# Kernel tuning notes

Measured on AMD Instinct MI355X. Metric: run time of the kernel, lower is better.

The kernel has to match this reference:

```python
import jax, jax.numpy as jnp
import numpy as np

EPS = 1e-5
K_SIZE, STRIDE, DILATION, N_HEADS = 8, 2, 2, 8


def ln2d(x, w, b):
    # LayerNorm2d: normalize over channel axis of NCHW
    m = x.mean(1, keepdims=True)
    v = x.var(1, keepdims=True)
    return (x - m) * jax.lax.rsqrt(v + EPS) * w[None, :, None, None] + b[None, :, None, None]


def setup_inputs() -> dict:
    key = jax.random.key(0)
    ks = jax.random.split(key, 8)
    B, C, H, W = 1, 64, 128, 128
    hid = 2 * C  # ffn_ratio = 2
    f = lambda k, s: jax.random.normal(k, s, jnp.float32) * 0.02
    return dict(
        x=jax.random.normal(ks[0], (B, C, H, W), jnp.float32),
        norm1_w=jnp.ones(C, jnp.float32), norm1_b=jnp.zeros(C, jnp.float32),
        qkv_w=f(ks[1], (3 * C, C)), qkv_b=jnp.zeros(3 * C, jnp.float32),
        qn_w=jnp.ones(C, jnp.float32), qn_b=jnp.zeros(C, jnp.float32),
        kn_w=jnp.ones(C, jnp.float32), kn_b=jnp.zeros(C, jnp.float32),
        proj_w=f(ks[2], (C, C)), proj_b=jnp.zeros(C, jnp.float32),
        gamma1=jnp.full((C,), 0.1, jnp.float32),
        norm2_w=jnp.ones(C, jnp.float32), norm2_b=jnp.zeros(C, jnp.float32),
        fc1_w=f(ks[3], (hid, C)), fc1_b=jnp.zeros(hid, jnp.float32),
        mn_w=jnp.ones(hid, jnp.float32), mn_b=jnp.zeros(hid, jnp.float32),
        fc2_w=f(ks[4], (C, hid)), fc2_b=jnp.zeros(C, jnp.float32),
        gamma2=jnp.full((C,), 0.1, jnp.float32),
    )


def reference(x, norm1_w, norm1_b, qkv_w, qkv_b, qn_w, qn_b, kn_w, kn_b,
              proj_w, proj_b, gamma1, norm2_w, norm2_b,
              fc1_w, fc1_b, mn_w, mn_b, fc2_w, fc2_b, gamma2):
    B, C, H, W = x.shape
    n = N_HEADS
    hd = C // n
    # strided + dilated neighborhood offsets (includes 0 at center)
    off = (jnp.arange(K_SIZE) * STRIDE - (K_SIZE * STRIDE) // 2) * DILATION

    # ---- neighborhood attention branch ----
    xn = ln2d(x, norm1_w, norm1_b)
    qkv = jnp.einsum('oc,bchw->bohw', qkv_w, xn) + qkv_b[None, :, None, None]
    q, k, v = jnp.split(qkv, 3, axis=1)
    q = ln2d(q, qn_w, qn_b)
    k = ln2d(k, kn_w, kn_b)
    q = q.reshape(B, n, hd, H, W)
    k = k.reshape(B, n, hd, H, W)
    v = v.reshape(B, n, hd, H, W)

    pos_h = jnp.arange(H)[:, None] + off[None, :]            # [H, k]
    vh = (pos_h >= 0) & (pos_h < H)
    ih = jnp.clip(pos_h, 0, H - 1)
    pos_w = jnp.arange(W)[:, None] + off[None, :]            # [W, k]
    vw = (pos_w >= 0) & (pos_w < W)
    iw = jnp.clip(pos_w, 0, W - 1)

    # gather neighborhoods: [B,n,hd,H,kh,W,kw]
    Kg = jnp.take(jnp.take(k, ih, axis=3), iw, axis=5)
    Vg = jnp.take(jnp.take(v, ih, axis=3), iw, axis=5)

    scores = jnp.einsum('bnchw,bnchiwj->bnhwij', q, Kg) * (hd ** -0.5)
    mask = vh[:, None, :, None] & vw[None, :, None, :]        # [H,W,kh,kw]
    scores = jnp.where(mask[None, None], scores, -jnp.inf)
    a = jax.nn.softmax(scores.reshape(B, n, H, W, -1), axis=-1).reshape(scores.shape)
    o = jnp.einsum('bnhwij,bnchiwj->bnchw', a, Vg).reshape(B, C, H, W)
    o = jnp.einsum('oc,bchw->bohw', proj_w, o) + proj_b[None, :, None, None]
    x = x + gamma1[None, :, None, None] * o                  # ls1 + residual (drop_path=0)

    # ---- ConvMlp branch: 1x1 conv -> norm -> silu -> 1x1 conv ----
    y = ln2d(x, norm2_w, norm2_b)
    h1 = jnp.einsum('oc,bchw->bohw', fc1_w, y) + fc1_b[None, :, None, None]
    h1 = jax.nn.silu(ln2d(h1, mn_w, mn_b))
    h2 = jnp.einsum('oc,bchw->bohw', fc2_w, h1) + fc2_b[None, :, None, None]
    return x + gamma2[None, :, None, None] * h2
```

## Files before the change

kernel.cpp:

```cpp
#include <hip/hip_runtime.h>
#include <math.h>

#define HW 16384
#define CC 64
#define HID 128
#define EPSV 1e-5f
#define ROW 36
#define SROW 69
#define HDSTR 131072

typedef __attribute__((ext_vector_type(8))) short bf16x8;
typedef __attribute__((ext_vector_type(4))) float f32x4v;

__device__ __forceinline__ unsigned short f2bf(float f) {
    unsigned u = __float_as_uint(f);
    u += 0x7FFFu + ((u >> 16) & 1u);
    return (unsigned short)(u >> 16);
}
__device__ __forceinline__ unsigned pack2bf(float a, float b) {
    return (unsigned)f2bf(a) | ((unsigned)f2bf(b) << 16);
}


__global__ __launch_bounds__(256) void k_ln_qkv(
    const float* __restrict__ x,
    const float* __restrict__ n1w, const float* __restrict__ n1b,
    const float* __restrict__ qkvw, const float* __restrict__ qkvb,
    const float* __restrict__ qnw, const float* __restrict__ qnb,
    const float* __restrict__ knw, const float* __restrict__ knb,
    float* __restrict__ qo, float* __restrict__ ko, float* __restrict__ vo)
{
    __shared__ __align__(16) float xs[CC][ROW];
    __shared__ __align__(16) float qk[32][SROW];
    __shared__ __align__(16) float mu1[32], rs1[32], mu2[32], rs2[32];

    const int t = threadIdx.x;
    const int pix0 = blockIdx.x * 32;
    const int sel = blockIdx.y;

    {
        const int c = t >> 2, pxq = (t & 3) * 8;
        *(float4*)&xs[c][pxq]     = *(const float4*)(x + c * HW + pix0 + pxq);
        *(float4*)&xs[c][pxq + 4] = *(const float4*)(x + c * HW + pix0 + pxq + 4);
    }
    __syncthreads();

    if (t < 128) {
        const int px = ((t >> 6) << 4) + (t & 15);
        const int part = (t & 63) >> 4;
        float s = 0.f, ss = 0.f;
        #pragma unroll
        for (int i = 0; i < 16; ++i) { float v = xs[part * 16 + i][px]; s += v; ss += v * v; }
        s += __shfl_xor(s, 16); ss += __shfl_xor(ss, 16);
        s += __shfl_xor(s, 32); ss += __shfl_xor(ss, 32);
        if (part == 0) {
            float m = s * (1.f / CC);
            mu1[px] = m;
            rs1[px] = rsqrtf(ss * (1.f / CC) - m * m + EPSV);
        }
    }
    __syncthreads();

    {
        const int c = t >> 2, pxq = (t & 3) * 8;
        const float wgt = n1w[c], bia = n1b[c];
        #pragma unroll
        for (int hh = 0; hh < 2; ++hh) {
            float4 v = *(float4*)&xs[c][pxq + hh * 4];
            float4 m4 = *(float4*)&mu1[pxq + hh * 4];
            float4 r4 = *(float4*)&rs1[pxq + hh * 4];
            v.x = (v.x - m4.x) * r4.x * wgt + bia;
            v.y = (v.y - m4.y) * r4.y * wgt + bia;
            v.z = (v.z - m4.z) * r4.z * wgt + bia;
            v.w = (v.w - m4.w) * r4.w * wgt + bia;
            *(float4*)&xs[c][pxq + hh * 4] = v;
        }
    }
    __syncthreads();

    {
        const int o0 = (t >> 3) * 2;
        const int px0 = (t & 7) * 4;
        const int ow = sel * 64 + o0;
        float a[2][4];
        #pragma unroll
        for (int j = 0; j < 2; ++j) {
            float b = qkvb[ow + j];
            a[j][0] = b; a[j][1] = b; a[j][2] = b; a[j][3] = b;
        }
        for (int c = 0; c < CC; c += 4) {
            float4 xv[4];
            #pragma unroll
            for (int i = 0; i < 4; ++i) xv[i] = *(float4*)&xs[c + i][px0];
            #pragma unroll
            for (int j = 0; j < 2; ++j) {
                float4 wv = *(const float4*)(qkvw + (ow + j) * CC + c);
                #pragma unroll
                for (int pp = 0; pp < 4; ++pp) {
                    a[j][pp] += wv.x * (&xv[0].x)[pp] + wv.y * (&xv[1].x)[pp]
                              + wv.z * (&xv[2].x)[pp] + wv.w * (&xv[3].x)[pp];
                }
            }
        }
        #pragma unroll
        for (int j = 0; j < 2; ++j) {
            #pragma unroll
            for (int pp = 0; pp < 4; ++pp) qk[px0 + pp][o0 + j] = a[j][pp];
        }
    }
    __syncthreads();

    if (sel < 2) {
        if (t < 128) {
            const int px = ((t >> 6) << 4) + (t & 15);
            const int part = (t & 63) >> 4;
            float s = 0.f, ss = 0.f;
            #pragma unroll
            for (int i = 0; i < 16; ++i) { float v = qk[px][part * 16 + i]; s += v; ss += v * v; }
            s += __shfl_xor(s, 16); ss += __shfl_xor(ss, 16);
            s += __shfl_xor(s, 32); ss += __shfl_xor(ss, 32);
            if (part == 0) {
                float m = s * (1.f / CC);
                mu2[px] = m;
                rs2[px] = rsqrtf(ss * (1.f / CC) - m * m + EPSV);
            }
        }
        __syncthreads();
    }

    const float* lw = (sel == 0) ? qnw : knw;
    const float* lb = (sel == 0) ? qnb : knb;
    float* dst = (sel == 0) ? qo : ((sel == 1) ? ko : vo);
    #pragma unroll
    for (int pass = 0; pass < 2; ++pass) {
        const int px = (t >> 4) + pass * 16;
        const int cg = t & 15;
        const int c = cg * 4;
        const int hd = cg >> 1;
        const int d4 = (cg & 1) * 4;
        const int pixel = pix0 + px;
        const int h = pixel >> 7, w = pixel & 127;
        const int pos = ((h >> 2) * 32 + (w >> 2)) * 16 + (h & 3) * 4 + (w & 3);
        const int gbase = hd * HDSTR + pos * 8 + d4;

        float4 vv = *(float4*)&qk[px][c];
        if (sel < 2) {
            const float mm = mu2[px], rr = rs2[px];
            float4 w4 = *(const float4*)(lw + c);
            float4 b4 = *(const float4*)(lb + c);
            vv.x = (vv.x - mm) * rr * w4.x + b4.x;
            vv.y = (vv.y - mm) * rr * w4.y + b4.y;
            vv.z = (vv.z - mm) * rr * w4.z + b4.z;
            vv.w = (vv.w - mm) * rr * w4.w + b4.w;
        }
        *(float4*)(dst + gbase) = vv;
    }
}

__global__ __launch_bounds__(256) void k_attn(
    const float* __restrict__ q, const float* __restrict__ k, const float* __restrict__ v,
    float* __restrict__ o,
    const float* __restrict__ pw, const float* __restrict__ f1w, const float* __restrict__ f2w,
    unsigned short* __restrict__ pwh, unsigned short* __restrict__ f1h,
    unsigned short* __restrict__ f2h)
{
    __shared__ __align__(16) float kt[4][15][33][2];
    __shared__ __align__(16) float vt[4][15][33][2];

    const int t = threadIdx.x;
    const int band = blockIdx.x;
    const int sub  = blockIdx.y;
    const int head = blockIdx.z;
    const int hs0 = band * 8;

    {
        const int gtid = ((blockIdx.z * 16 + blockIdx.y) * 4 + blockIdx.x) * 256 + t;
        if (gtid < 4096)        pwh[gtid] = f2bf(pw[gtid]);
        else if (gtid < 12288)  f1h[gtid - 4096] = f2bf(f1w[gtid - 4096]);
        else if (gtid < 20480)  f2h[gtid - 12288] = f2bf(f2w[gtid - 12288]);
    }

    const float* kb = k + head * HDSTR;
    const float* vb = v + head * HDSTR;

    for (int idx = t; idx < 960; idx += 256) {
        const int row = idx >> 6;
        const int rem = idx & 63;
        const int wsc = rem >> 1;
        const int dh = rem & 1;
        int gr = hs0 - 4 + row;
        gr = gr < 0 ? 0 : (gr > 31 ? 31 : gr);
        const int gaddr = ((gr * 32 + wsc) * 16 + sub) * 8 + dh * 4;
        const float4 kv4 = *(const float4*)(kb + gaddr);
        const float4 vv4 = *(const float4*)(vb + gaddr);
        const int dp = dh * 2;
        kt[dp][row][wsc][0] = kv4.x;     kt[dp][row][wsc][1] = kv4.y;
        kt[dp + 1][row][wsc][0] = kv4.z; kt[dp + 1][row][wsc][1] = kv4.w;
        vt[dp][row][wsc][0] = vv4.x;     vt[dp][row][wsc][1] = vv4.y;
        vt[dp + 1][row][wsc][0] = vv4.z; vt[dp + 1][row][wsc][1] = vv4.w;
    }

    const int r = t >> 5;
    const int wsc = t & 31;
    const int hs = hs0 + r;

    const float* qp = q + head * HDSTR + ((hs * 32 + wsc) * 16 + sub) * 8;
    const float4 q0 = *(const float4*)qp;
    const float4 q1 = *(const float4*)(qp + 4);
    const float scale = 0.35355339059327373f;

    __syncthreads();

    float s[64];
    float mx0 = -1e30f, mx1 = -1e30f, mx2 = -1e30f, mx3 = -1e30f;
    #pragma unroll
    for (int i = 0; i < 8; ++i) {
        const int lr = r + i;
        const bool vh = (unsigned)(hs + i - 4) < 32u;
        #pragma unroll
        for (int j = 0; j < 8; ++j) {
            const int cs = wsc + j - 4;
            const bool valid = vh && ((unsigned)cs < 32u);
            const int cc = cs < 0 ? 0 : (cs > 31 ? 31 : cs);
            const float2 kA = *(const float2*)&kt[0][lr][cc][0];
            const float2 kB = *(const float2*)&kt[1][lr][cc][0];
            const float2 kC = *(const float2*)&kt[2][lr][cc][0];
            const float2 kD = *(const float2*)&kt[3][lr][cc][0];
            float sv = q0.x * kA.x + q0.y * kA.y + q0.z * kB.x + q0.w * kB.y
                     + q1.x * kC.x + q1.y * kC.y + q1.z * kD.x + q1.w * kD.y;
            sv *= scale;
            sv = valid ? sv : -INFINITY;
            s[i * 8 + j] = sv;
            if ((j & 3) == 0)      mx0 = fmaxf(mx0, sv);
            else if ((j & 3) == 1) mx1 = fmaxf(mx1, sv);
            else if ((j & 3) == 2) mx2 = fmaxf(mx2, sv);
            else                   mx3 = fmaxf(mx3, sv);
        }
    }
    const float mx = fmaxf(fmaxf(mx0, mx1), fmaxf(mx2, mx3));

    float l = 0.f;
    float a0 = 0.f, a1 = 0.f, a2 = 0.f, a3 = 0.f, a4 = 0.f, a5 = 0.f, a6 = 0.f, a7 = 0.f;
    #pragma unroll
    for (int i = 0; i < 8; ++i) {
        const int lr = r + i;
        #pragma unroll
        for (int j = 0; j < 8; ++j) {
            const int cs = wsc + j - 4;
            const int cc = cs < 0 ? 0 : (cs > 31 ? 31 : cs);
            const float p = __expf(s[i * 8 + j] - mx);
            const float2 vA = *(const float2*)&vt[0][lr][cc][0];
            const float2 vB = *(const float2*)&vt[1][lr][cc][0];
            const float2 vC = *(const float2*)&vt[2][lr][cc][0];
            const float2 vD = *(const float2*)&vt[3][lr][cc][0];
            l += p;
            a0 += p * vA.x;  a1 += p * vA.y;
            a2 += p * vB.x;  a3 += p * vB.y;
            a4 += p * vC.x;  a5 += p * vC.y;
            a6 += p * vD.x;  a7 += p * vD.y;
        }
    }

    const float inv = 1.f / l;
    const int a = sub >> 2, b = sub & 3;
    const int h = hs * 4 + a, w = wsc * 4 + b;
    float* op = o + (h * 128 + w) * 64 + head * 8;
    float4 r0 = {a0 * inv, a1 * inv, a2 * inv, a3 * inv};
    float4 r1 = {a4 * inv, a5 * inv, a6 * inv, a7 * inv};
    *(float4*)op = r0;
    *(float4*)(op + 4) = r1;
}

__global__ __launch_bounds__(256) void k_mlp(
    const float* __restrict__ x, const float* __restrict__ oatt,
    const unsigned short* __restrict__ pwh, const float* __restrict__ pb,
    const float* __restrict__ g1,
    const float* __restrict__ n2w, const float* __restrict__ n2b,
    const unsigned short* __restrict__ f1h, const float* __restrict__ f1b,
    const float* __restrict__ mnw, const float* __restrict__ mnb,
    const unsigned short* __restrict__ f2h, const float* __restrict__ f2b,
    const float* __restrict__ g2,
    float* __restrict__ out)
{
    __shared__ __align__(16) float xres[CC][ROW];
    __shared__ __align__(16) unsigned short oh[32][72];
    __shared__ __align__(16) unsigned short tbh[32][72];
    __shared__ __align__(16) float h1[HID][ROW];
    __shared__ __align__(16) unsigned short h1h[32][136];
    __shared__ __align__(16) float mu[32], rs[32];

    const int t = threadIdx.x;
    const int pix0 = blockIdx.x * 32;
    const int wv = t >> 6;
    const int l = t & 63;
    const int ln = l & 15;
    const int kg = l >> 4;

    {
        const int c = t >> 2, pxq = (t & 3) * 8;
        *(float4*)&xres[c][pxq]     = *(const float4*)(x + c * HW + pix0 + pxq);
        *(float4*)&xres[c][pxq + 4] = *(const float4*)(x + c * HW + pix0 + pxq + 4);
    }
    #pragma unroll
    for (int pass = 0; pass < 2; ++pass) {
        const int px = (t >> 4) + pass * 16, cg = (t & 15) * 4;
        float4 ov = *(const float4*)(oatt + (pix0 + px) * CC + cg);
        *(unsigned*)&oh[px][cg]     = pack2bf(ov.x, ov.y);
        *(unsigned*)&oh[px][cg + 2] = pack2bf(ov.z, ov.w);
    }
    __syncthreads();

    {
        f32x4v acc0 = {0.f, 0.f, 0.f, 0.f}, acc1 = {0.f, 0.f, 0.f, 0.f};
        const int m = wv * 16 + ln;
        #pragma unroll
        for (int kk = 0; kk < 64; kk += 32) {
            const int k0 = kk + kg * 8;
            bf16x8 av = *(const bf16x8*)(pwh + m * 64 + k0);
            bf16x8 b0 = *(const bf16x8*)&oh[ln][k0];
            bf16x8 b1 = *(const bf16x8*)&oh[16 + ln][k0];
            acc0 = __builtin_amdgcn_mfma_f32_16x16x32_bf16(av, b0, acc0, 0, 0, 0);
            acc1 = __builtin_amdgcn_mfma_f32_16x16x32_bf16(av, b1, acc1, 0, 0, 0);
        }
        const int r0 = wv * 16 + kg * 4;
        float4 pb4 = *(const float4*)(pb + r0);
        float4 g14 = *(const float4*)(g1 + r0);
        #pragma unroll
        for (int reg = 0; reg < 4; ++reg) {
            const int row = r0 + reg;
            xres[row][ln]      += (&g14.x)[reg] * (acc0[reg] + (&pb4.x)[reg]);
            xres[row][16 + ln] += (&g14.x)[reg] * (acc1[reg] + (&pb4.x)[reg]);
        }
    }
    __syncthreads();

    if (t < 128) {
        const int px = ((t >> 6) << 4) + (t & 15);
        const int part = (t & 63) >> 4;
        float s = 0.f, ss = 0.f;
        #pragma unroll
        for (int i = 0; i < 16; ++i) { float v = xres[part * 16 + i][px]; s += v; ss += v * v; }
        s += __shfl_xor(s, 16); ss += __shfl_xor(ss, 16);
        s += __shfl_xor(s, 32); ss += __shfl_xor(ss, 32);
        if (part == 0) {
            float m = s * (1.f / CC);
            mu[px] = m;
            rs[px] = rsqrtf(ss * (1.f / CC) - m * m + EPSV);
        }
    }
    __syncthreads();

    {
        const int c2 = (t & 31) * 2, px0 = (t >> 5) * 4;
        const float w0 = n2w[c2], b0 = n2b[c2];
        const float w1 = n2w[c2 + 1], b1 = n2b[c2 + 1];
        float4 va = *(float4*)&xres[c2][px0];
        float4 vb = *(float4*)&xres[c2 + 1][px0];
        float4 m4 = *(float4*)&mu[px0];
        float4 r4 = *(float4*)&rs[px0];
        #pragma unroll
        for (int i = 0; i < 4; ++i) {
            float f0 = ((&va.x)[i] - (&m4.x)[i]) * (&r4.x)[i] * w0 + b0;
            float f1 = ((&vb.x)[i] - (&m4.x)[i]) * (&r4.x)[i] * w1 + b1;
            *(unsigned*)&tbh[px0 + i][c2] = pack2bf(f0, f1);
        }
    }
    __syncthreads();

    {
        f32x4v a00 = {0.f,0.f,0.f,0.f}, a01 = {0.f,0.f,0.f,0.f};
        f32x4v a10 = {0.f,0.f,0.f,0.f}, a11 = {0.f,0.f,0.f,0.f};
        const int m0 = wv * 32 + ln;
        #pragma unroll
        for (int kk = 0; kk < 64; kk += 32) {
            const int k0 = kk + kg * 8;
            bf16x8 av0 = *(const bf16x8*)(f1h + m0 * 64 + k0);
            bf16x8 av1 = *(const bf16x8*)(f1h + (m0 + 16) * 64 + k0);
            bf16x8 b0 = *(const bf16x8*)&tbh[ln][k0];
            bf16x8 b1 = *(const bf16x8*)&tbh[16 + ln][k0];
            a00 = __builtin_amdgcn_mfma_f32_16x16x32_bf16(av0, b0, a00, 0, 0, 0);
            a01 = __builtin_amdgcn_mfma_f32_16x16x32_bf16(av0, b1, a01, 0, 0, 0);
            a10 = __builtin_amdgcn_mfma_f32_16x16x32_bf16(av1, b0, a10, 0, 0, 0);
            a11 = __builtin_amdgcn_mfma_f32_16x16x32_bf16(av1, b1, a11, 0, 0, 0);
        }
        const int r0 = wv * 32 + kg * 4;
        float4 fb0 = *(const float4*)(f1b + r0);
        float4 fb1 = *(const float4*)(f1b + r0 + 16);
        #pragma unroll
        for (int reg = 0; reg < 4; ++reg) {
            h1[r0 + reg][ln]           = a00[reg] + (&fb0.x)[reg];
            h1[r0 + reg][16 + ln]      = a01[reg] + (&fb0.x)[reg];
            h1[r0 + 16 + reg][ln]      = a10[reg] + (&fb1.x)[reg];
            h1[r0 + 16 + reg][16 + ln] = a11[reg] + (&fb1.x)[reg];
        }
    }
    __syncthreads();

    if (t < 128) {
        const int px = ((t >> 6) << 4) + (t & 15);
        const int part = (t & 63) >> 4;
        float s = 0.f, ss = 0.f;
        #pragma unroll
        for (int i = 0; i < 32; ++i) { float v = h1[part * 32 + i][px]; s += v; ss += v * v; }
        s += __shfl_xor(s, 16); ss += __shfl_xor(ss, 16);
        s += __shfl_xor(s, 32); ss += __shfl_xor(ss, 32);
        if (part == 0) {
            float m = s * (1.f / HID);
            mu[px] = m;
            rs[px] = rsqrtf(ss * (1.f / HID) - m * m + EPSV);
        }
    }
    __syncthreads();

    {
        const int c2 = (t & 63) * 2, pxm = (t >> 6) * 8;
        const float w0 = mnw[c2], b0 = mnb[c2];
        const float w1 = mnw[c2 + 1], b1 = mnb[c2 + 1];
        #pragma unroll
        for (int qq = 0; qq < 2; ++qq) {
            float4 va = *(float4*)&h1[c2][pxm + qq * 4];
            float4 vb = *(float4*)&h1[c2 + 1][pxm + qq * 4];
            float4 m4 = *(float4*)&mu[pxm + qq * 4];
            float4 r4 = *(float4*)&rs[pxm + qq * 4];
            #pragma unroll
            for (int i = 0; i < 4; ++i) {
                float h0 = ((&va.x)[i] - (&m4.x)[i]) * (&r4.x)[i] * w0 + b0;
                float h1v = ((&vb.x)[i] - (&m4.x)[i]) * (&r4.x)[i] * w1 + b1;
                h0 = h0 / (1.f + __expf(-h0));
                h1v = h1v / (1.f + __expf(-h1v));
                *(unsigned*)&h1h[pxm + qq * 4 + i][c2] = pack2bf(h0, h1v);
            }
        }
    }
    __syncthreads();

    {
        f32x4v acc0 = {0.f, 0.f, 0.f, 0.f}, acc1 = {0.f, 0.f, 0.f, 0.f};
        const int m = wv * 16 + ln;
        #pragma unroll
        for (int kk = 0; kk < 128; kk += 32) {
            const int k0 = kk + kg * 8;
            bf16x8 av = *(const bf16x8*)(f2h + m * 128 + k0);
            bf16x8 b0 = *(const bf16x8*)&h1h[ln][k0];
            bf16x8 b1 = *(const bf16x8*)&h1h[16 + ln][k0];
            acc0 = __builtin_amdgcn_mfma_f32_16x16x32_bf16(av, b0, acc0, 0, 0, 0);
            acc1 = __builtin_amdgcn_mfma_f32_16x16x32_bf16(av, b1, acc1, 0, 0, 0);
        }
        const int r0 = wv * 16 + kg * 4;
        float4 fb4 = *(const float4*)(f2b + r0);
        float4 g24 = *(const float4*)(g2 + r0);
        #pragma unroll
        for (int reg = 0; reg < 4; ++reg) {
            const int row = r0 + reg;
            out[row * HW + pix0 + ln]      = xres[row][ln]
                                           + (&g24.x)[reg] * (acc0[reg] + (&fb4.x)[reg]);
            out[row * HW + pix0 + 16 + ln] = xres[row][16 + ln]
                                           + (&g24.x)[reg] * (acc1[reg] + (&fb4.x)[reg]);
        }
    }
}

extern "C" void kernel_launch(void* const* d_in, const int* in_sizes, int n_in,
                              void* d_out, int out_size, void* d_ws, size_t ws_size,
                              hipStream_t stream) {
    (void)in_sizes; (void)n_in; (void)out_size; (void)ws_size;
    const float* x      = (const float*)d_in[0];
    const float* n1w    = (const float*)d_in[1];
    const float* n1b    = (const float*)d_in[2];
    const float* qkvw   = (const float*)d_in[3];
    const float* qkvb   = (const float*)d_in[4];
    const float* qnw    = (const float*)d_in[5];
    const float* qnb    = (const float*)d_in[6];
    const float* knw    = (const float*)d_in[7];
    const float* knb    = (const float*)d_in[8];
    const float* pw     = (const float*)d_in[9];
    const float* pb     = (const float*)d_in[10];
    const float* g1     = (const float*)d_in[11];
    const float* n2w    = (const float*)d_in[12];
    const float* n2b    = (const float*)d_in[13];
    const float* f1w    = (const float*)d_in[14];
    const float* f1b    = (const float*)d_in[15];
    const float* mnw    = (const float*)d_in[16];
    const float* mnb    = (const float*)d_in[17];
    const float* f2w    = (const float*)d_in[18];
    const float* f2b    = (const float*)d_in[19];
    const float* g2     = (const float*)d_in[20];
    float* out = (float*)d_out;

    float* ws = (float*)d_ws;
    const size_t CHW = (size_t)CC * HW;
    float* qo   = ws;
    float* ko   = ws + CHW;
    float* vo   = ws + 2 * CHW;
    float* oatt = ws + 3 * CHW;
    unsigned short* wsh = (unsigned short*)(ws + 4 * CHW);
    unsigned short* pwh = wsh;
    unsigned short* f1h = wsh + 4096;
    unsigned short* f2h = wsh + 12288;

    k_ln_qkv<<<dim3(HW / 32, 3), dim3(256), 0, stream>>>(
        x, n1w, n1b, qkvw, qkvb, qnw, qnb, knw, knb, qo, ko, vo);
    k_attn<<<dim3(4, 16, 8), dim3(256), 0, stream>>>(
        qo, ko, vo, oatt, pw, f1w, f2w, pwh, f1h, f2h);
    k_mlp<<<dim3(HW / 32), dim3(256), 0, stream>>>(
        x, oatt, pwh, pb, g1, n2w, n2b, f1h, f1b, mnw, mnb, f2h, f2b, g2, out);
}
```

Before: 135.8 us.

## Compute QKV projection with bf16 MFMA in one block per pixel tile

The QKV kernel now computes all three 64-channel outputs in a single block rather than one block per q/k/v selector, so LayerNorm1 and the x tile load are no longer repeated three times. The 1x1 projection moves from fp32 FMA loops to bf16 MFMA 16x16x32 instructions, with weights and normalized activations converted to bf16 in shared memory. Both q and k LayerNorms run concurrently on separate halves of the block. The cost is more shared memory per block, lower occupancy, per-block weight conversion, and reduced precision in the projection.

```diff
diff --git a/kernel.cpp b/kernel.cpp
--- a/kernel.cpp
+++ b/kernel.cpp
@@ -6,7 +6,7 @@
 #define HID 128
 #define EPSV 1e-5f
 #define ROW 36
-#define SROW 69
+#define QROW 197
 #define HDSTR 131072
 
 typedef __attribute__((ext_vector_type(8))) short bf16x8;
@@ -31,17 +31,31 @@
     float* __restrict__ qo, float* __restrict__ ko, float* __restrict__ vo)
 {
     __shared__ __align__(16) float xs[CC][ROW];
-    __shared__ __align__(16) float qk[32][SROW];
-    __shared__ __align__(16) float mu1[32], rs1[32], mu2[32], rs2[32];
+    __shared__ __align__(16) unsigned short xh[32][72];
+    __shared__ __align__(16) unsigned short wh[192][72];
+    __shared__ __align__(16) float qk[32][QROW];
+    __shared__ __align__(16) float mu1[32], rs1[32], muq[32], rsq[32], muk[32], rsk[32];
 
     const int t = threadIdx.x;
     const int pix0 = blockIdx.x * 32;
-    const int sel = blockIdx.y;
+    const int wv = t >> 6;
+    const int l = t & 63;
+    const int ln = l & 15;
+    const int kg = l >> 4;
 
     {
         const int c = t >> 2, pxq = (t & 3) * 8;
         *(float4*)&xs[c][pxq]     = *(const float4*)(x + c * HW + pix0 + pxq);
         *(float4*)&xs[c][pxq + 4] = *(const float4*)(x + c * HW + pix0 + pxq + 4);
+    }
+    #pragma unroll
+    for (int i = 0; i < 12; ++i) {
+        const int f = i * 256 + t;
+        const int row = f >> 4;
+        const int k4 = (f & 15) * 4;
+        float4 wv4 = *(const float4*)(qkvw + row * 64 + k4);
+        *(unsigned*)&wh[row][k4]     = pack2bf(wv4.x, wv4.y);
+        *(unsigned*)&wh[row][k4 + 2] = pack2bf(wv4.z, wv4.w);
     }
     __syncthreads();
 
@@ -62,75 +76,85 @@
     __syncthreads();
 
     {
-        const int c = t >> 2, pxq = (t & 3) * 8;
-        const float wgt = n1w[c], bia = n1b[c];
-        #pragma unroll
-        for (int hh = 0; hh < 2; ++hh) {
-            float4 v = *(float4*)&xs[c][pxq + hh * 4];
-            float4 m4 = *(float4*)&mu1[pxq + hh * 4];
-            float4 r4 = *(float4*)&rs1[pxq + hh * 4];
-            v.x = (v.x - m4.x) * r4.x * wgt + bia;
-            v.y = (v.y - m4.y) * r4.y * wgt + bia;
-            v.z = (v.z - m4.z) * r4.z * wgt + bia;
-            v.w = (v.w - m4.w) * r4.w * wgt + bia;
-            *(float4*)&xs[c][pxq + hh * 4] = v;
-        }
-    }
-    __syncthreads();
-
-    {
-        const int o0 = (t >> 3) * 2;
-        const int px0 = (t & 7) * 4;
-        const int ow = sel * 64 + o0;
-        float a[2][4];
-        #pragma unroll
-        for (int j = 0; j < 2; ++j) {
-            float b = qkvb[ow + j];
-            a[j][0] = b; a[j][1] = b; a[j][2] = b; a[j][3] = b;
-        }
-        for (int c = 0; c < CC; c += 4) {
-            float4 xv[4];
+        const int c2 = (t & 31) * 2, px0 = (t >> 5) * 4;
+        const float w0 = n1w[c2], b0 = n1b[c2];
+        const float w1 = n1w[c2 + 1], b1 = n1b[c2 + 1];
+        float4 va = *(float4*)&xs[c2][px0];
+        float4 vb = *(float4*)&xs[c2 + 1][px0];
+        float4 m4 = *(float4*)&mu1[px0];
+        float4 r4 = *(float4*)&rs1[px0];
+        #pragma unroll
+        for (int i = 0; i < 4; ++i) {
+            float f0 = ((&va.x)[i] - (&m4.x)[i]) * (&r4.x)[i] * w0 + b0;
+            float f1 = ((&vb.x)[i] - (&m4.x)[i]) * (&r4.x)[i] * w1 + b1;
+            *(unsigned*)&xh[px0 + i][c2] = pack2bf(f0, f1);
+        }
+    }
+    __syncthreads();
+
+    {
+        f32x4v acc[3][2];
+        #pragma unroll
+        for (int mt = 0; mt < 3; ++mt) {
+            acc[mt][0] = (f32x4v){0.f, 0.f, 0.f, 0.f};
+            acc[mt][1] = (f32x4v){0.f, 0.f, 0.f, 0.f};
+        }
+        const int mbase = wv * 48;
+        #pragma unroll
+        for (int kk = 0; kk < 64; kk += 32) {
+            const int k0 = kk + kg * 8;
+            bf16x8 b0 = *(const bf16x8*)&xh[ln][k0];
+            bf16x8 b1 = *(const bf16x8*)&xh[16 + ln][k0];
             #pragma unroll
-            for (int i = 0; i < 4; ++i) xv[i] = *(float4*)&xs[c + i][px0];
+            for (int mt = 0; mt < 3; ++mt) {
+                bf16x8 av = *(const bf16x8*)&wh[mbase + mt * 16 + ln][k0];
+                acc[mt][0] = __builtin_amdgcn_mfma_f32_16x16x32_bf16(av, b0, acc[mt][0], 0, 0, 0);
+                acc[mt][1] = __builtin_amdgcn_mfma_f32_16x16x32_bf16(av, b1, acc[mt][1], 0, 0, 0);
+            }
+        }
+        #pragma unroll
+        for (int mt = 0; mt < 3; ++mt) {
+            const int r0 = mbase + mt * 16 + kg * 4;
+            float4 qb4 = *(const float4*)(qkvb + r0);
             #pragma unroll
-            for (int j = 0; j < 2; ++j) {
-                float4 wv = *(const float4*)(qkvw + (ow + j) * CC + c);
-                #pragma unroll
-                for (int pp = 0; pp < 4; ++pp) {
-                    a[j][pp] += wv.x * (&xv[0].x)[pp] + wv.y * (&xv[1].x)[pp]
-                              + wv.z * (&xv[2].x)[pp] + wv.w * (&xv[3].x)[pp];
-                }
+            for (int reg = 0; reg < 4; ++reg) {
+                qk[ln][r0 + reg]      = acc[mt][0][reg] + (&qb4.x)[reg];
+                qk[16 + ln][r0 + reg] = acc[mt][1][reg] + (&qb4.x)[reg];
             }
         }
-        #pragma unroll
-        for (int j = 0; j < 2; ++j) {
-            #pragma unroll
-            for (int pp = 0; pp < 4; ++pp) qk[px0 + pp][o0 + j] = a[j][pp];
-        }
-    }
-    __syncthreads();
-
-    if (sel < 2) {
-        if (t < 128) {
-            const int px = ((t >> 6) << 4) + (t & 15);
-            const int part = (t & 63) >> 4;
-            float s = 0.f, ss = 0.f;
-            #pragma unroll
-            for (int i = 0; i < 16; ++i) { float v = qk[px][part * 16 + i]; s += v; ss += v * v; }
-            s += __shfl_xor(s, 16); ss += __shfl_xor(ss, 16);
-            s += __shfl_xor(s, 32); ss += __shfl_xor(ss, 32);
-            if (part == 0) {
-                float m = s * (1.f / CC);
-                mu2[px] = m;
-                rs2[px] = rsqrtf(ss * (1.f / CC) - m * m + EPSV);
-            }
-        }
-        __syncthreads();
-    }
-
-    const float* lw = (sel == 0) ? qnw : knw;
-    const float* lb = (sel == 0) ? qnb : knb;
-    float* dst = (sel == 0) ? qo : ((sel == 1) ? ko : vo);
+    }
+    __syncthreads();
+
+    if (t < 128) {
+        const int px = ((t >> 6) << 4) + (t & 15);
+        const int part = (t & 63) >> 4;
+        float s = 0.f, ss = 0.f;
+        #pragma unroll
+        for (int i = 0; i < 16; ++i) { float v = qk[px][part * 16 + i]; s += v; ss += v * v; }
+        s += __shfl_xor(s, 16); ss += __shfl_xor(ss, 16);
+        s += __shfl_xor(s, 32); ss += __shfl_xor(ss, 32);
+        if (part == 0) {
+            float m = s * (1.f / CC);
+            muq[px] = m;
+            rsq[px] = rsqrtf(ss * (1.f / CC) - m * m + EPSV);
+        }
+    } else {
+        const int t2 = t - 128;
+        const int px = ((t2 >> 6) << 4) + (t2 & 15);
+        const int part = (t2 & 63) >> 4;
+        float s = 0.f, ss = 0.f;
+        #pragma unroll
+        for (int i = 0; i < 16; ++i) { float v = qk[px][CC + part * 16 + i]; s += v; ss += v * v; }
+        s += __shfl_xor(s, 16); ss += __shfl_xor(ss, 16);
+        s += __shfl_xor(s, 32); ss += __shfl_xor(ss, 32);
+        if (part == 0) {
+            float m = s * (1.f / CC);
+            muk[px] = m;
+            rsk[px] = rsqrtf(ss * (1.f / CC) - m * m + EPSV);
+        }
+    }
+    __syncthreads();
+
     #pragma unroll
     for (int pass = 0; pass < 2; ++pass) {
         const int px = (t >> 4) + pass * 16;
@@ -143,17 +167,28 @@
         const int pos = ((h >> 2) * 32 + (w >> 2)) * 16 + (h & 3) * 4 + (w & 3);
         const int gbase = hd * HDSTR + pos * 8 + d4;
 
-        float4 vv = *(float4*)&qk[px][c];
-        if (sel < 2) {
-            const float mm = mu2[px], rr = rs2[px];
-            float4 w4 = *(const float4*)(lw + c);
-            float4 b4 = *(const float4*)(lb + c);
-            vv.x = (vv.x - mm) * rr * w4.x + b4.x;
-            vv.y = (vv.y - mm) * rr * w4.y + b4.y;
-            vv.z = (vv.z - mm) * rr * w4.z + b4.z;
-            vv.w = (vv.w - mm) * rr * w4.w + b4.w;
-        }
-        *(float4*)(dst + gbase) = vv;
+        const float mq = muq[px], rq = rsq[px];
+        float4 qv = *(float4*)&qk[px][c];
+        float4 qw = *(const float4*)(qnw + c);
+        float4 qb = *(const float4*)(qnb + c);
+        qv.x = (qv.x - mq) * rq * qw.x + qb.x;
+        qv.y = (qv.y - mq) * rq * qw.y + qb.y;
+        qv.z = (qv.z - mq) * rq * qw.z + qb.z;
+        qv.w = (qv.w - mq) * rq * qw.w + qb.w;
+        *(float4*)(qo + gbase) = qv;
+
+        const float mk = muk[px], rk = rsk[px];
+        float4 kv = *(float4*)&qk[px][CC + c];
+        float4 kw = *(const float4*)(knw + c);
+        float4 kb = *(const float4*)(knb + c);
+        kv.x = (kv.x - mk) * rk * kw.x + kb.x;
+        kv.y = (kv.y - mk) * rk * kw.y + kb.y;
+        kv.z = (kv.z - mk) * rk * kw.z + kb.z;
+        kv.w = (kv.w - mk) * rk * kw.w + kb.w;
+        *(float4*)(ko + gbase) = kv;
+
+        float4 vv = *(float4*)&qk[px][2 * CC + c];
+        *(float4*)(vo + gbase) = vv;
     }
 }
 
@@ -498,7 +533,7 @@
     unsigned short* f1h = wsh + 4096;
     unsigned short* f2h = wsh + 12288;
 
-    k_ln_qkv<<<dim3(HW / 32, 3), dim3(256), 0, stream>>>(
+    k_ln_qkv<<<dim3(HW / 32), dim3(256), 0, stream>>>(
         x, n1w, n1b, qkvw, qkvb, qnw, qnb, knw, knb, qo, ko, vo);
     k_attn<<<dim3(4, 16, 8), dim3(256), 0, stream>>>(
         qo, ko, vo, oatt, pw, f1w, f2w, pwh, f1h, f2h);
```

Measured after the change: 131.6 us. 3.1% less time.
